# Kernel optimization log

Hardware: AMD Instinct MI355X
Metric: run time of the kernel (lower is better)

The kernel has to match this reference:

```python
import jax, jax.numpy as jnp
import numpy as np

N_NODES = 50000
N_EDGES = 1600000
IN_CH = 128
HEADS = 4
HEAD_DIM = 32  # out_channels // heads = 128 // 4
NEG_SLOPE = 0.2


def setup_inputs() -> dict:
    key = jax.random.key(0)
    ks = jax.random.split(key, 6)
    x = jax.random.normal(ks[0], (N_NODES, IN_CH), dtype=jnp.float32)
    edge_index = jax.random.randint(ks[1], (2, N_EDGES), 0, N_NODES, dtype=jnp.int64)
    W = jax.random.normal(ks[2], (IN_CH, HEADS * HEAD_DIM), dtype=jnp.float32) * 0.1
    att_src = jax.random.normal(ks[3], (HEADS, HEAD_DIM), dtype=jnp.float32) * 0.1
    att_dst = jax.random.normal(ks[4], (HEADS, HEAD_DIM), dtype=jnp.float32) * 0.1
    bias = jax.random.normal(ks[5], (HEADS * HEAD_DIM,), dtype=jnp.float32) * 0.1
    return {"x": x, "edge_index": edge_index, "W": W,
            "att_src": att_src, "att_dst": att_dst, "bias": bias}


def reference(x, edge_index, W, att_src, att_dst, bias):
    N = x.shape[0]
    # linear projection, split heads: [N, H, C]
    h = (x @ W).reshape(N, HEADS, HEAD_DIM)
    # per-node attention logits: [N, H]
    a_src = jnp.einsum('nhc,hc->nh', h, att_src)
    a_dst = jnp.einsum('nhc,hc->nh', h, att_dst)
    # add self loops (PyG default)
    loops = jnp.arange(N, dtype=edge_index.dtype)
    src = jnp.concatenate([edge_index[0], loops])  # message source j
    dst = jnp.concatenate([edge_index[1], loops])  # message target i
    # edge attention scores: [E_total, H]
    alpha = jax.nn.leaky_relu(a_src[src] + a_dst[dst], NEG_SLOPE)
    # segment softmax over incoming edges per destination node
    amax = jax.ops.segment_max(alpha, dst, num_segments=N)
    alpha = jnp.exp(alpha - amax[dst])
    denom = jax.ops.segment_sum(alpha, dst, num_segments=N)
    alpha = alpha / (denom[dst] + 1e-16)
    # weighted scatter-aggregate: [N, H, C]
    msg = h[src] * alpha[:, :, None]
    out = jax.ops.segment_sum(msg, dst, num_segments=N)
    out = out.reshape(N, HEADS * HEAD_DIM) + bias
    return jax.nn.elu(out)
```

## Files before the change

kernel.cpp:

```cpp
#include <hip/hip_runtime.h>

typedef unsigned short u16;
typedef unsigned int u32;

#define CH 128
#define NHEAD 4
#define NEG_SLOPE 0.2f
#define ROWS_PER_BLOCK 32

#define LOG_NPB 7
#define NPB 128
#define NBMAX 400
#define BCAP 6144
#define KMB 6
#define GPAD 16
#define BINA_BLOCKS 256

static __device__ __forceinline__ float bitf(u32 i) {
    float f; __builtin_memcpy(&f, &i, 4); return f;
}
static __device__ __forceinline__ float bflo(u32 v) { return bitf(v << 16); }
static __device__ __forceinline__ float bfhi(u32 v) { return bitf(v & 0xffff0000u); }
static __device__ __forceinline__ u16 f2bf(float f) {
    u32 i; __builtin_memcpy(&i, &f, 4);
    return (u16)((i + 0x7fffu + ((i >> 16) & 1u)) >> 16);
}
static __device__ __forceinline__ float lrelu(float v) { return v > 0.f ? v : NEG_SLOPE * v; }

static __device__ __forceinline__ int ei_at(const int* __restrict__ ei, int mode32, size_t idx) {
    return mode32 ? ei[idx] : ei[2 * idx];
}

__global__ __launch_bounds__(256) void gemmbin_kernel(
    const float* __restrict__ x, const float* __restrict__ W,
    const float* __restrict__ att_src, const float* __restrict__ att_dst,
    u16* __restrict__ h, float* __restrict__ asrc, float* __restrict__ adst, int N,
    const int* __restrict__ ei, int* __restrict__ gcur, u32* __restrict__ rec,
    int E, int NB)
{
    __shared__ float xs[ROWS_PER_BLOCK][CH];
    __shared__ u32 Wbf[CH][CH / 2];

    const int tid = threadIdx.x;

    if (blockIdx.x < BINA_BLOCKS) {
        int* hist  = (int*)&xs[0][0];
        int* hbase = hist + NBMAX;
        int* hcur  = hbase + NBMAX;
        const int mode32 = __syncthreads_or(ei[2 * tid + 1] != 0);
        for (int b = tid; b < NB; b += 256) { hist[b] = 0; hcur[b] = 0; }
        __syncthreads();
        const int chunk = (E + BINA_BLOCKS - 1) / BINA_BLOCKS;
        const int beg0 = blockIdx.x * chunk;
        const int end0 = min(E, beg0 + chunk);
#pragma unroll 4
        for (int e = beg0 + tid; e < end0; e += 256) {
            int dj = ei_at(ei, mode32, (size_t)E + e);
            atomicAdd(&hist[dj >> LOG_NPB], 1);
        }
        __syncthreads();
        for (int b = tid; b < NB; b += 256) {
            int c = hist[b];
            hbase[b] = c ? atomicAdd(&gcur[b * GPAD], c) : 0;
        }
        __syncthreads();
#pragma unroll 4
        for (int e = beg0 + tid; e < end0; e += 256) {
            int dj = ei_at(ei, mode32, (size_t)E + e);
            int sj = ei_at(ei, mode32, (size_t)e);
            int bkt = dj >> LOG_NPB;
            int r = atomicAdd(&hcur[bkt], 1);
            int pos = hbase[bkt] + r;
            if (pos < BCAP)
                rec[(size_t)bkt * BCAP + pos] = ((u32)sj << LOG_NPB) | (u32)(dj & (NPB - 1));
        }
        return;
    }

    const int gb = blockIdx.x - BINA_BLOCKS;
    const int r0b = gb * ROWS_PER_BLOCK;
    {
#pragma unroll
        for (int i = 0; i < 16; ++i) {
            int f = tid + i * 256;
            int row = f >> 5;
            int col = (f & 31) * 4;
            float4 w4 = *(const float4*)(W + (size_t)row * CH + col);
            Wbf[row][(col >> 1)]     = (u32)f2bf(w4.x) | ((u32)f2bf(w4.y) << 16);
            Wbf[row][(col >> 1) + 1] = (u32)f2bf(w4.z) | ((u32)f2bf(w4.w) << 16);
        }
#pragma unroll
        for (int i = 0; i < 4; ++i) {
            int f = tid + i * 256;
            int row = f >> 5;
            int col = (f & 31) * 4;
            if (r0b + row < N)
                *(float4*)&xs[row][col] = *(const float4*)(x + (size_t)(r0b + row) * CH + col);
        }
    }
    __syncthreads();

    const int lane = tid & 63;
    const int wave = tid >> 6;
    const int c0 = lane * 2;
    const int head = lane >> 4;
    const float as0 = att_src[c0], as1 = att_src[c0 + 1];
    const float ad0 = att_dst[c0], ad1 = att_dst[c0 + 1];
    const int rw = wave * 8;

    float acc[8][2];
#pragma unroll
    for (int r = 0; r < 8; ++r) { acc[r][0] = 0.f; acc[r][1] = 0.f; }

#pragma unroll 4
    for (int k4 = 0; k4 < 32; ++k4) {
        const int k = k4 * 4;
        u32 p0 = Wbf[k + 0][lane];
        u32 p1 = Wbf[k + 1][lane];
        u32 p2 = Wbf[k + 2][lane];
        u32 p3 = Wbf[k + 3][lane];
        float w00 = bflo(p0), w01 = bfhi(p0);
        float w10 = bflo(p1), w11 = bfhi(p1);
        float w20 = bflo(p2), w21 = bfhi(p2);
        float w30 = bflo(p3), w31 = bfhi(p3);
#pragma unroll
        for (int r = 0; r < 8; ++r) {
            float4 xv = *(const float4*)&xs[rw + r][k];
            acc[r][0] = fmaf(xv.x, w00, acc[r][0]);
            acc[r][1] = fmaf(xv.x, w01, acc[r][1]);
            acc[r][0] = fmaf(xv.y, w10, acc[r][0]);
            acc[r][1] = fmaf(xv.y, w11, acc[r][1]);
            acc[r][0] = fmaf(xv.z, w20, acc[r][0]);
            acc[r][1] = fmaf(xv.z, w21, acc[r][1]);
            acc[r][0] = fmaf(xv.w, w30, acc[r][0]);
            acc[r][1] = fmaf(xv.w, w31, acc[r][1]);
        }
    }
#pragma unroll
    for (int r = 0; r < 8; ++r) {
        int row = r0b + rw + r;
        float sdot = acc[r][0] * as0 + acc[r][1] * as1;
        float ddot = acc[r][0] * ad0 + acc[r][1] * ad1;
#pragma unroll
        for (int o = 1; o < 16; o <<= 1) {
            sdot += __shfl_xor(sdot, o, 64);
            ddot += __shfl_xor(ddot, o, 64);
        }
        if (row < N) {
            u32 hp = (u32)f2bf(acc[r][0]) | ((u32)f2bf(acc[r][1]) << 16);
            *(u32*)(h + (size_t)row * CH + c0) = hp;
            if ((lane & 15) == 0) {
                asrc[row * NHEAD + head] = sdot;
                adst[row * NHEAD + head] = ddot;
            }
        }
    }
}

__global__ __launch_bounds__(1024) void binBagg_kernel(
    const u16* __restrict__ h, const float* __restrict__ asrc, const float* __restrict__ adst,
    const int* __restrict__ gcur, const u32* __restrict__ rec,
    const float* __restrict__ bias, float* __restrict__ out, int N)
{
    __shared__ int outb[BCAP + 32];
    __shared__ int lcnt[NPB];
    __shared__ int lsc[NPB];
    __shared__ int lcur[NPB];
    const int tid = threadIdx.x;
    const int bkt = blockIdx.x;
    int cnt0 = gcur[bkt * GPAD];
    cnt0 = cnt0 < BCAP ? cnt0 : BCAP;
    const size_t rbase = (size_t)bkt * BCAP;

    if (tid < NPB) { lcnt[tid] = 0; lcur[tid] = 0; }

    u32 rc[KMB];
#pragma unroll
    for (int k = 0; k < KMB; ++k) {
        int i = tid + k * 1024;
        rc[k] = (i < cnt0) ? rec[rbase + i] : 0xffffffffu;
    }
    __syncthreads();
#pragma unroll
    for (int k = 0; k < KMB; ++k)
        if (rc[k] != 0xffffffffu) atomicAdd(&lcnt[rc[k] & (NPB - 1)], 1);
    __syncthreads();
    if (tid < NPB) lsc[tid] = lcnt[tid];
    __syncthreads();
    for (int o = 1; o < NPB; o <<= 1) {
        int v = (tid < NPB && tid >= o) ? lsc[tid - o] : 0;
        __syncthreads();
        if (tid < NPB) lsc[tid] += v;
        __syncthreads();
    }
#pragma unroll
    for (int k = 0; k < KMB; ++k) {
        if (rc[k] != 0xffffffffu) {
            int local = rc[k] & (NPB - 1);
            int r = atomicAdd(&lcur[local], 1);
            int slot = (lsc[local] - lcnt[local]) + r;
            outb[slot] = (int)(rc[k] >> LOG_NPB);
        }
    }
    __syncthreads();

    const int lane = tid & 63;
    const int wave = tid >> 6;
    const int g = lane >> 4;
    const int l = lane & 15;
    const int c8 = l * 8;
    const int head = l >> 2;

    for (int nl = 0; nl < 8; ++nl) {
        const int local = wave * 8 + nl;
        const int node = (bkt << LOG_NPB) + local;
        if (node >= N) continue;
        const int beg = lsc[local] - lcnt[local];
        const int end = lsc[local];
        const float4 ad4 = *(const float4*)(adst + node * 4);
        const float adh = (head == 0) ? ad4.x : (head == 1) ? ad4.y : (head == 2) ? ad4.z : ad4.w;
        const float4 asl = *(const float4*)(asrc + node * 4);
        const float aslh = (head == 0) ? asl.x : (head == 1) ? asl.y : (head == 2) ? asl.z : asl.w;
        const float mh = lrelu(aslh + adh);

        float acc[8];
#pragma unroll
        for (int k = 0; k < 8; ++k) acc[k] = 0.f;
        float s = 0.f;

        int e = beg + g;
        if (e < end) {
            uint4 hC[4]; float aC[4];
#pragma unroll
            for (int i = 0; i < 4; ++i) {
                int ei = e + 4 * i;
                int j = outb[ei];
                j = ((u32)j < (u32)N) ? j : 0;
                float a = asrc[j * NHEAD + head];
                aC[i] = (ei < end) ? a : -1e30f;
                hC[i] = *(const uint4*)(h + (size_t)j * CH + c8);
            }
            for (;;) {
                const int ebase = e + 16;
                uint4 hP[4]; float aP[4];
#pragma unroll
                for (int i = 0; i < 4; ++i) {
                    int ei = ebase + 4 * i;
                    int j = outb[ei];
                    j = ((u32)j < (u32)N) ? j : 0;
                    float a = asrc[j * NHEAD + head];
                    aP[i] = (ei < end) ? a : -1e30f;
                    hP[i] = *(const uint4*)(h + (size_t)j * CH + c8);
                }
#pragma unroll
                for (int i = 0; i < 4; ++i) {
                    float w = __expf(lrelu(aC[i] + adh) - mh);
                    s += w;
                    acc[0] = fmaf(w, bflo(hC[i].x), acc[0]);
                    acc[1] = fmaf(w, bfhi(hC[i].x), acc[1]);
                    acc[2] = fmaf(w, bflo(hC[i].y), acc[2]);
                    acc[3] = fmaf(w, bfhi(hC[i].y), acc[3]);
                    acc[4] = fmaf(w, bflo(hC[i].z), acc[4]);
                    acc[5] = fmaf(w, bfhi(hC[i].z), acc[5]);
                    acc[6] = fmaf(w, bflo(hC[i].w), acc[6]);
                    acc[7] = fmaf(w, bfhi(hC[i].w), acc[7]);
                }
#pragma unroll
                for (int i = 0; i < 4; ++i) { aC[i] = aP[i]; hC[i] = hP[i]; }
                e = ebase;
                if (e >= end) break;
            }
        }
        if (g == 0) {
            s += 1.0f;
            uint4 hv = *(const uint4*)(h + (size_t)node * CH + c8);
            acc[0] += bflo(hv.x);
            acc[1] += bfhi(hv.x);
            acc[2] += bflo(hv.y);
            acc[3] += bfhi(hv.y);
            acc[4] += bflo(hv.z);
            acc[5] += bfhi(hv.z);
            acc[6] += bflo(hv.w);
            acc[7] += bfhi(hv.w);
        }
#pragma unroll
        for (int o = 16; o < 64; o <<= 1) {
            s += __shfl_xor(s, o, 64);
#pragma unroll
            for (int k = 0; k < 8; ++k) acc[k] += __shfl_xor(acc[k], o, 64);
        }
        if (g == 0) {
            const float inv = 1.f / (s + 1e-16f);
            float o0[8];
#pragma unroll
            for (int k = 0; k < 8; ++k) {
                float v = acc[k] * inv + bias[c8 + k];
                o0[k] = v > 0.f ? v : __expf(v) - 1.f;
            }
            float4 lo = make_float4(o0[0], o0[1], o0[2], o0[3]);
            float4 hi = make_float4(o0[4], o0[5], o0[6], o0[7]);
            *(float4*)(out + (size_t)node * CH + c8) = lo;
            *(float4*)(out + (size_t)node * CH + c8 + 4) = hi;
        }
    }
}

extern "C" void kernel_launch(void* const* d_in, const int* in_sizes, int n_in,
                              void* d_out, int out_size, void* d_ws, size_t ws_size,
                              hipStream_t stream)
{
    const float* x       = (const float*)d_in[0];
    const int*   ei      = (const int*)d_in[1];
    const float* W       = (const float*)d_in[2];
    const float* att_src = (const float*)d_in[3];
    const float* att_dst = (const float*)d_in[4];
    const float* bias    = (const float*)d_in[5];
    float* out = (float*)d_out;
    const int N = in_sizes[0] / CH;
    const int E = in_sizes[1] / 2;
    const int NB = (N + NPB - 1) / NPB;

    char* p = (char*)d_ws;
    auto alloc = [&](size_t bytes) { char* r = p; p += (bytes + 255) & ~(size_t)255; return r; };
    u16*   h    = (u16*)alloc((size_t)N * CH * 2);
    float* asrc = (float*)alloc((size_t)N * NHEAD * 4);
    float* adst = (float*)alloc((size_t)N * NHEAD * 4);
    int*   gcur = (int*)alloc((size_t)NB * GPAD * 4);
    u32*   rec  = (u32*)alloc((size_t)NB * BCAP * 4);

    const int gemmBlocks = (N + ROWS_PER_BLOCK - 1) / ROWS_PER_BLOCK;
    hipMemsetAsync(gcur, 0, (size_t)NB * GPAD * 4, stream);
    gemmbin_kernel<<<BINA_BLOCKS + gemmBlocks, 256, 0, stream>>>(
        x, W, att_src, att_dst, h, asrc, adst, N, ei, gcur, rec, E, NB);
    binBagg_kernel<<<NB, 1024, 0, stream>>>(h, asrc, adst, gcur, rec, bias, out, N);
}
```

Baseline: 200.5 us.

## Split aggregation buckets across two blocks and precompute bf16 weights once

The aggregation kernel now launches two 512-thread blocks per 128-node bucket. Each block reads the whole bucket's records but keeps only its 64-node half, giving more, smaller blocks with less shared memory each. A small init kernel converts W to bf16 once and zeroes the counters, replacing the memset and the per-GEMM-block conversion so GEMM blocks only copy packed weights. The cost is that every bucket's records are read twice, and there is a new HCAP cap of 4096 edges per half-bucket, which could truncate edges if a half-bucket overflows.

```diff
diff --git a/kernel.cpp b/kernel.cpp
--- a/kernel.cpp
+++ b/kernel.cpp
@@ -12,7 +12,8 @@
 #define NPB 128
 #define NBMAX 400
 #define BCAP 6144
-#define KMB 6
+#define HCAP 4096
+#define KMB 12
 #define GPAD 16
 #define BINA_BLOCKS 256
 
@@ -31,8 +32,18 @@
     return mode32 ? ei[idx] : ei[2 * idx];
 }
 
+__global__ __launch_bounds__(256) void init_kernel(
+    const float* __restrict__ W, u32* __restrict__ Wg, int* __restrict__ gcur, int nGcur)
+{
+    const int t = blockIdx.x * 256 + threadIdx.x;
+    float4 w4 = ((const float4*)W)[t];
+    Wg[2 * t]     = (u32)f2bf(w4.x) | ((u32)f2bf(w4.y) << 16);
+    Wg[2 * t + 1] = (u32)f2bf(w4.z) | ((u32)f2bf(w4.w) << 16);
+    for (int i = t; i < nGcur; i += 4096) gcur[i] = 0;
+}
+
 __global__ __launch_bounds__(256) void gemmbin_kernel(
-    const float* __restrict__ x, const float* __restrict__ W,
+    const float* __restrict__ x, const u32* __restrict__ Wg,
     const float* __restrict__ att_src, const float* __restrict__ att_dst,
     u16* __restrict__ h, float* __restrict__ asrc, float* __restrict__ adst, int N,
     const int* __restrict__ ei, int* __restrict__ gcur, u32* __restrict__ rec,
@@ -80,14 +91,12 @@
     const int gb = blockIdx.x - BINA_BLOCKS;
     const int r0b = gb * ROWS_PER_BLOCK;
     {
-#pragma unroll
-        for (int i = 0; i < 16; ++i) {
+        const uint4* Wg4 = (const uint4*)Wg;
+        uint4* Wb4 = (uint4*)&Wbf[0][0];
+#pragma unroll
+        for (int i = 0; i < 8; ++i) {
             int f = tid + i * 256;
-            int row = f >> 5;
-            int col = (f & 31) * 4;
-            float4 w4 = *(const float4*)(W + (size_t)row * CH + col);
-            Wbf[row][(col >> 1)]     = (u32)f2bf(w4.x) | ((u32)f2bf(w4.y) << 16);
-            Wbf[row][(col >> 1) + 1] = (u32)f2bf(w4.z) | ((u32)f2bf(w4.w) << 16);
+            Wb4[f] = Wg4[f];
         }
 #pragma unroll
         for (int i = 0; i < 4; ++i) {
@@ -157,49 +166,54 @@
     }
 }
 
-__global__ __launch_bounds__(1024) void binBagg_kernel(
+__global__ __launch_bounds__(512) void binBagg_kernel(
     const u16* __restrict__ h, const float* __restrict__ asrc, const float* __restrict__ adst,
     const int* __restrict__ gcur, const u32* __restrict__ rec,
     const float* __restrict__ bias, float* __restrict__ out, int N)
 {
-    __shared__ int outb[BCAP + 32];
-    __shared__ int lcnt[NPB];
-    __shared__ int lsc[NPB];
-    __shared__ int lcur[NPB];
+    __shared__ int outb[HCAP + 32];
+    __shared__ int lcnt[64];
+    __shared__ int lsc[64];
+    __shared__ int lcur[64];
     const int tid = threadIdx.x;
-    const int bkt = blockIdx.x;
+    const int bkt  = blockIdx.x >> 1;
+    const int half = blockIdx.x & 1;
     int cnt0 = gcur[bkt * GPAD];
     cnt0 = cnt0 < BCAP ? cnt0 : BCAP;
     const size_t rbase = (size_t)bkt * BCAP;
 
-    if (tid < NPB) { lcnt[tid] = 0; lcur[tid] = 0; }
+    if (tid < 64) { lcnt[tid] = 0; lcur[tid] = 0; }
 
     u32 rc[KMB];
 #pragma unroll
     for (int k = 0; k < KMB; ++k) {
-        int i = tid + k * 1024;
+        int i = tid + k * 512;
         rc[k] = (i < cnt0) ? rec[rbase + i] : 0xffffffffu;
     }
     __syncthreads();
 #pragma unroll
-    for (int k = 0; k < KMB; ++k)
-        if (rc[k] != 0xffffffffu) atomicAdd(&lcnt[rc[k] & (NPB - 1)], 1);
-    __syncthreads();
-    if (tid < NPB) lsc[tid] = lcnt[tid];
-    __syncthreads();
-    for (int o = 1; o < NPB; o <<= 1) {
-        int v = (tid < NPB && tid >= o) ? lsc[tid - o] : 0;
-        __syncthreads();
-        if (tid < NPB) lsc[tid] += v;
-        __syncthreads();
-    }
-#pragma unroll
     for (int k = 0; k < KMB; ++k) {
-        if (rc[k] != 0xffffffffu) {
-            int local = rc[k] & (NPB - 1);
-            int r = atomicAdd(&lcur[local], 1);
-            int slot = (lsc[local] - lcnt[local]) + r;
-            outb[slot] = (int)(rc[k] >> LOG_NPB);
+        u32 r = rc[k];
+        if (r != 0xffffffffu && (int)((r & 127) >> 6) == half)
+            atomicAdd(&lcnt[r & 63], 1);
+    }
+    __syncthreads();
+    if (tid < 64) lsc[tid] = lcnt[tid];
+    __syncthreads();
+    for (int o = 1; o < 64; o <<= 1) {
+        int v = (tid < 64 && tid >= o) ? lsc[tid - o] : 0;
+        __syncthreads();
+        if (tid < 64) lsc[tid] += v;
+        __syncthreads();
+    }
+#pragma unroll
+    for (int k = 0; k < KMB; ++k) {
+        u32 r = rc[k];
+        if (r != 0xffffffffu && (int)((r & 127) >> 6) == half) {
+            int local = r & 63;
+            int rr = atomicAdd(&lcur[local], 1);
+            int slot = (lsc[local] - lcnt[local]) + rr;
+            if (slot < HCAP) outb[slot] = (int)(r >> LOG_NPB);
         }
     }
     __syncthreads();
@@ -213,10 +227,11 @@
 
     for (int nl = 0; nl < 8; ++nl) {
         const int local = wave * 8 + nl;
-        const int node = (bkt << LOG_NPB) + local;
+        const int node = (bkt << LOG_NPB) + half * 64 + local;
         if (node >= N) continue;
-        const int beg = lsc[local] - lcnt[local];
-        const int end = lsc[local];
+        int end = lsc[local];
+        const int beg = end - lcnt[local];
+        end = end < HCAP ? end : HCAP;
         const float4 ad4 = *(const float4*)(adst + node * 4);
         const float adh = (head == 0) ? ad4.x : (head == 1) ? ad4.y : (head == 2) ? ad4.z : ad4.w;
         const float4 asl = *(const float4*)(asrc + node * 4);
@@ -327,10 +342,11 @@
     float* adst = (float*)alloc((size_t)N * NHEAD * 4);
     int*   gcur = (int*)alloc((size_t)NB * GPAD * 4);
     u32*   rec  = (u32*)alloc((size_t)NB * BCAP * 4);
+    u32*   Wg   = (u32*)alloc((size_t)CH * CH / 2 * 4);
 
     const int gemmBlocks = (N + ROWS_PER_BLOCK - 1) / ROWS_PER_BLOCK;
-    hipMemsetAsync(gcur, 0, (size_t)NB * GPAD * 4, stream);
+    init_kernel<<<16, 256, 0, stream>>>(W, Wg, gcur, NB * GPAD);
     gemmbin_kernel<<<BINA_BLOCKS + gemmBlocks, 256, 0, stream>>>(
-        x, W, att_src, att_dst, h, asrc, adst, N, ei, gcur, rec, E, NB);
-    binBagg_kernel<<<NB, 1024, 0, stream>>>(h, asrc, adst, gcur, rec, bias, out, N);
-}
+        x, Wg, att_src, att_dst, h, asrc, adst, N, ei, gcur, rec, E, NB);
+    binBagg_kernel<<<2 * NB, 512, 0, stream>>>(h, asrc, adst, gcur, rec, bias, out, N);
+}
```

Measured after the change: 216.4 us. 1.08x slower.

## Use bf16 MFMA with split-precision x for projection GEMM, preswizzle W

Applied to the files above, without the earlier changes.

Replaces the scalar FMA projection GEMM with MFMA 16x16x32 bf16 instructions. x is split into hi and lo bf16 parts to keep accuracy close to fp32. A new init kernel pre-converts W once into an MFMA-ready swizzled bf16 layout and also zeroes the bucket counters, replacing the memset. The h tile is staged through LDS so it can be written out in coalesced rows. This costs two MFMAs per tile and an extra small kernel launch.

```diff
diff --git a/kernel.cpp b/kernel.cpp
--- a/kernel.cpp
+++ b/kernel.cpp
@@ -7,6 +7,7 @@
 #define NHEAD 4
 #define NEG_SLOPE 0.2f
 #define ROWS_PER_BLOCK 32
+#define XPAD 132
 
 #define LOG_NPB 7
 #define NPB 128
@@ -16,6 +17,9 @@
 #define GPAD 16
 #define BINA_BLOCKS 256
 
+typedef __attribute__((ext_vector_type(8))) short bf16x8;
+typedef __attribute__((ext_vector_type(4))) float f32x4;
+
 static __device__ __forceinline__ float bitf(u32 i) {
     float f; __builtin_memcpy(&f, &i, 4); return f;
 }
@@ -31,15 +35,39 @@
     return mode32 ? ei[idx] : ei[2 * idx];
 }
 
+__global__ __launch_bounds__(256) void init_kernel(
+    const float* __restrict__ W, uint4* __restrict__ Wsw, int* __restrict__ gcur, int nGcur)
+{
+    const int t = blockIdx.x * 256 + threadIdx.x;
+    if (t < 2048) {
+        const int lane = t & 63, ks = (t >> 6) & 3, nt = t >> 8;
+        const int col = nt * 16 + (lane & 15);
+        const int kb = ks * 32 + ((lane >> 4) << 2);
+        u16 v[8];
+#pragma unroll
+        for (int j = 0; j < 8; ++j) {
+            int kk = kb + (j & 3) + ((j >> 2) << 4);
+            v[j] = f2bf(W[(size_t)kk * CH + col]);
+        }
+        uint4 q;
+        q.x = (u32)v[0] | ((u32)v[1] << 16);
+        q.y = (u32)v[2] | ((u32)v[3] << 16);
+        q.z = (u32)v[4] | ((u32)v[5] << 16);
+        q.w = (u32)v[6] | ((u32)v[7] << 16);
+        Wsw[t] = q;
+    }
+    for (int i = t; i < nGcur; i += 4096) gcur[i] = 0;
+}
+
 __global__ __launch_bounds__(256) void gemmbin_kernel(
-    const float* __restrict__ x, const float* __restrict__ W,
+    const float* __restrict__ x, const uint4* __restrict__ Wsw,
     const float* __restrict__ att_src, const float* __restrict__ att_dst,
     u16* __restrict__ h, float* __restrict__ asrc, float* __restrict__ adst, int N,
     const int* __restrict__ ei, int* __restrict__ gcur, u32* __restrict__ rec,
     int E, int NB)
 {
-    __shared__ float xs[ROWS_PER_BLOCK][CH];
-    __shared__ u32 Wbf[CH][CH / 2];
+    __shared__ float xs[ROWS_PER_BLOCK][XPAD];
+    __shared__ uint4 Wb[2048];
 
     const int tid = threadIdx.x;
 
@@ -79,80 +107,96 @@
 
     const int gb = blockIdx.x - BINA_BLOCKS;
     const int r0b = gb * ROWS_PER_BLOCK;
+#pragma unroll
+    for (int i = 0; i < 8; ++i) Wb[tid + i * 256] = Wsw[tid + i * 256];
+#pragma unroll
+    for (int i = 0; i < 4; ++i) {
+        int f = tid + i * 256;
+        int row = f >> 5;
+        int col = (f & 31) * 4;
+        if (r0b + row < N)
+            *(float4*)&xs[row][col] = *(const float4*)(x + (size_t)(r0b + row) * CH + col);
+    }
+    __syncthreads();
+
+    const int lane = tid & 63;
+    const int w = tid >> 6;
+    const int g = lane >> 4;
+    const int a15 = lane & 15;
+    const int rt = w & 1;
+    const int cb4 = w >> 1;
+
+    f32x4 acc[4] = {};
+
+#pragma unroll
+    for (int ks = 0; ks < 4; ++ks) {
+        const float* xr = &xs[rt * 16 + a15][ks * 32 + g * 4];
+        float4 av0 = *(const float4*)xr;
+        float4 av1 = *(const float4*)(xr + 16);
+        float av[8] = {av0.x, av0.y, av0.z, av0.w, av1.x, av1.y, av1.z, av1.w};
+        bf16x8 ahi, alo;
+#pragma unroll
+        for (int j = 0; j < 8; ++j) {
+            u16 hb = f2bf(av[j]);
+            ahi[j] = (short)hb;
+            alo[j] = (short)f2bf(av[j] - bflo(hb));
+        }
+#pragma unroll
+        for (int ct = 0; ct < 4; ++ct) {
+            bf16x8 b = *(const bf16x8*)&Wb[((cb4 * 4 + ct) * 4 + ks) * 64 + lane];
+            acc[ct] = __builtin_amdgcn_mfma_f32_16x16x32_bf16(alo, b, acc[ct], 0, 0, 0);
+            acc[ct] = __builtin_amdgcn_mfma_f32_16x16x32_bf16(ahi, b, acc[ct], 0, 0, 0);
+        }
+    }
+
+    float as_c[4], ad_c[4];
+#pragma unroll
+    for (int ct = 0; ct < 4; ++ct) {
+        int c = cb4 * 64 + ct * 16 + a15;
+        as_c[ct] = att_src[c];
+        ad_c[ct] = att_dst[c];
+    }
+#pragma unroll
+    for (int i = 0; i < 4; ++i) {
+        float s0 = acc[0][i] * as_c[0] + acc[1][i] * as_c[1];
+        float s1 = acc[2][i] * as_c[2] + acc[3][i] * as_c[3];
+        float d0 = acc[0][i] * ad_c[0] + acc[1][i] * ad_c[1];
+        float d1 = acc[2][i] * ad_c[2] + acc[3][i] * ad_c[3];
+#pragma unroll
+        for (int o = 1; o < 16; o <<= 1) {
+            s0 += __shfl_xor(s0, o, 64);
+            s1 += __shfl_xor(s1, o, 64);
+            d0 += __shfl_xor(d0, o, 64);
+            d1 += __shfl_xor(d1, o, 64);
+        }
+        if (a15 == 0) {
+            int row = r0b + rt * 16 + g * 4 + i;
+            if (row < N) {
+                int hb0 = cb4 * 2;
+                asrc[row * NHEAD + hb0]     = s0;
+                asrc[row * NHEAD + hb0 + 1] = s1;
+                adst[row * NHEAD + hb0]     = d0;
+                adst[row * NHEAD + hb0 + 1] = d1;
+            }
+        }
+    }
+
+    __syncthreads();
+    u16* ht = (u16*)&xs[0][0];
+#pragma unroll
+    for (int ct = 0; ct < 4; ++ct)
+#pragma unroll
+        for (int i = 0; i < 4; ++i)
+            ht[(rt * 16 + g * 4 + i) * CH + cb4 * 64 + ct * 16 + a15] = f2bf(acc[ct][i]);
+    __syncthreads();
     {
-#pragma unroll
-        for (int i = 0; i < 16; ++i) {
-            int f = tid + i * 256;
-            int row = f >> 5;
-            int col = (f & 31) * 4;
-            float4 w4 = *(const float4*)(W + (size_t)row * CH + col);
-            Wbf[row][(col >> 1)]     = (u32)f2bf(w4.x) | ((u32)f2bf(w4.y) << 16);
-            Wbf[row][(col >> 1) + 1] = (u32)f2bf(w4.z) | ((u32)f2bf(w4.w) << 16);
-        }
-#pragma unroll
-        for (int i = 0; i < 4; ++i) {
-            int f = tid + i * 256;
-            int row = f >> 5;
-            int col = (f & 31) * 4;
-            if (r0b + row < N)
-                *(float4*)&xs[row][col] = *(const float4*)(x + (size_t)(r0b + row) * CH + col);
-        }
-    }
-    __syncthreads();
-
-    const int lane = tid & 63;
-    const int wave = tid >> 6;
-    const int c0 = lane * 2;
-    const int head = lane >> 4;
-    const float as0 = att_src[c0], as1 = att_src[c0 + 1];
-    const float ad0 = att_dst[c0], ad1 = att_dst[c0 + 1];
-    const int rw = wave * 8;
-
-    float acc[8][2];
-#pragma unroll
-    for (int r = 0; r < 8; ++r) { acc[r][0] = 0.f; acc[r][1] = 0.f; }
-
-#pragma unroll 4
-    for (int k4 = 0; k4 < 32; ++k4) {
-        const int k = k4 * 4;
-        u32 p0 = Wbf[k + 0][lane];
-        u32 p1 = Wbf[k + 1][lane];
-        u32 p2 = Wbf[k + 2][lane];
-        u32 p3 = Wbf[k + 3][lane];
-        float w00 = bflo(p0), w01 = bfhi(p0);
-        float w10 = bflo(p1), w11 = bfhi(p1);
-        float w20 = bflo(p2), w21 = bfhi(p2);
-        float w30 = bflo(p3), w31 = bfhi(p3);
+        const u32* ht32 = (const u32*)&xs[0][0];
+        const int rw = w * 8;
 #pragma unroll
         for (int r = 0; r < 8; ++r) {
-            float4 xv = *(const float4*)&xs[rw + r][k];
-            acc[r][0] = fmaf(xv.x, w00, acc[r][0]);
-            acc[r][1] = fmaf(xv.x, w01, acc[r][1]);
-            acc[r][0] = fmaf(xv.y, w10, acc[r][0]);
-            acc[r][1] = fmaf(xv.y, w11, acc[r][1]);
-            acc[r][0] = fmaf(xv.z, w20, acc[r][0]);
-            acc[r][1] = fmaf(xv.z, w21, acc[r][1]);
-            acc[r][0] = fmaf(xv.w, w30, acc[r][0]);
-            acc[r][1] = fmaf(xv.w, w31, acc[r][1]);
-        }
-    }
-#pragma unroll
-    for (int r = 0; r < 8; ++r) {
-        int row = r0b + rw + r;
-        float sdot = acc[r][0] * as0 + acc[r][1] * as1;
-        float ddot = acc[r][0] * ad0 + acc[r][1] * ad1;
-#pragma unroll
-        for (int o = 1; o < 16; o <<= 1) {
-            sdot += __shfl_xor(sdot, o, 64);
-            ddot += __shfl_xor(ddot, o, 64);
-        }
-        if (row < N) {
-            u32 hp = (u32)f2bf(acc[r][0]) | ((u32)f2bf(acc[r][1]) << 16);
-            *(u32*)(h + (size_t)row * CH + c0) = hp;
-            if ((lane & 15) == 0) {
-                asrc[row * NHEAD + head] = sdot;
-                adst[row * NHEAD + head] = ddot;
-            }
+            int row = r0b + rw + r;
+            if (row < N)
+                *(u32*)(h + (size_t)row * CH + lane * 2) = ht32[(rw + r) * 64 + lane];
         }
     }
 }
@@ -327,10 +371,11 @@
     float* adst = (float*)alloc((size_t)N * NHEAD * 4);
     int*   gcur = (int*)alloc((size_t)NB * GPAD * 4);
     u32*   rec  = (u32*)alloc((size_t)NB * BCAP * 4);
+    uint4* Wsw  = (uint4*)alloc((size_t)2048 * 16);
 
     const int gemmBlocks = (N + ROWS_PER_BLOCK - 1) / ROWS_PER_BLOCK;
-    hipMemsetAsync(gcur, 0, (size_t)NB * GPAD * 4, stream);
+    init_kernel<<<16, 256, 0, stream>>>(W, Wsw, gcur, NB * GPAD);
     gemmbin_kernel<<<BINA_BLOCKS + gemmBlocks, 256, 0, stream>>>(
-        x, W, att_src, att_dst, h, asrc, adst, N, ei, gcur, rec, E, NB);
+        x, Wsw, att_src, att_dst, h, asrc, adst, N, ei, gcur, rec, E, NB);
     binBagg_kernel<<<NB, 1024, 0, stream>>>(h, asrc, adst, gcur, rec, bias, out, N);
 }
```

Result: no change. 197.3 us (-1.6%).
